# Kernel tuning notes

Hardware: AMD Instinct MI355X
Metric: run time of the kernel (lower is better)

Reference implementation:

```python
import jax, jax.numpy as jnp
import numpy as np

T_STEPS = 64   # rollout horizon (static for lax.scan)
DT = 0.1       # step(x, u) = x + DT*u (single-integrator dynamics)

def setup_inputs() -> dict:
    key = jax.random.key(0)
    k0, k1, k2, k3 = jax.random.split(key, 4)
    B, N, p, q, kgnn, fgnn = 64, 1024, 4, 4, 3, 32
    x0 = jax.random.normal(k0, (B, N, p), dtype=jnp.float32)
    # scale S so spectral norm ~O(1): matrix powers S^i stay bounded
    S = jax.random.normal(k1, (N, N), dtype=jnp.float32) / np.float32(np.sqrt(N))
    H1 = jax.random.normal(k2, (kgnn + 1, p, fgnn), dtype=jnp.float32)
    H2 = jax.random.normal(k3, (1, fgnn, q), dtype=jnp.float32)
    return {"x0": x0, "S": S, "H1": H1, "H2": H2}

def reference(x0, S, H1, H2):
    kgnn = H1.shape[0] - 1
    N = S.shape[0]
    # Precompute S^0..S^kgnn once (the torch code recomputes them every step)
    pows = [jnp.eye(N, dtype=S.dtype)]
    for _ in range(kgnn):
        pows.append(pows[-1] @ S)
    S_pows = jnp.stack(pows)  # (kgnn+1, N, N)

    def body(xt, _):
        # Z = tanh(sum_i S^i X H1[i]); each S^i @ X is a skinny matmul (inner dim p)
        SX = jnp.einsum('knm,bmp->kbnp', S_pows, xt)        # (k+1, B, N, p)
        Z = jnp.tanh(jnp.einsum('kbnp,kpf->bnf', SX, H1))   # (B, N, fgnn)
        U = jnp.einsum('nm,bmf,fq->bnq', S, Z, H2[0])       # (B, N, q)
        xn = xt + DT * U                                     # step(xt, ut)
        return xn, (xn, U)

    _, (xs, us) = jax.lax.scan(body, x0, None, length=T_STEPS)
    x_traj = jnp.concatenate([x0[:, None], jnp.moveaxis(xs, 0, 1)], axis=1)  # (B, T+1, N, p)
    u_traj = jnp.moveaxis(us, 0, 1)                                          # (B, T, N, q)
    return (x_traj, u_traj)
```

## Files before the change

kernel.cpp:

```cpp
#include <hip/hip_runtime.h>

#define T_STEPS 64
#define NN 1024
#define BKC 128

typedef __bf16 bf16x8 __attribute__((ext_vector_type(8)));
typedef float f32x4 __attribute__((ext_vector_type(4)));

__device__ __forceinline__ float fast_tanh(float z) {
    z = fminf(15.f, fmaxf(-15.f, z));
    const float t = __builtin_amdgcn_exp2f(z * 2.8853900817779268f);
    return (t - 1.f) * __builtin_amdgcn_rcpf(t + 1.f);
}

__global__ __launch_bounds__(512, 1) void step_kernel(
    const __bf16* __restrict__ AF,
    const __bf16* __restrict__ WFh, const __bf16* __restrict__ WFl,
    __bf16* __restrict__ WFoh, __bf16* __restrict__ WFol,
    float* __restrict__ SX, float* __restrict__ x_traj, float* __restrict__ u_traj,
    const float* __restrict__ H1, const float* __restrict__ H2, int t)
{
    __shared__ __align__(16) float dumps[8][4096];
    __shared__ float h1s[512];
    __shared__ float h2s[128];

    const int tid  = threadIdx.x;
    const int lane = tid & 63;
    const int w    = tid >> 6;

    h1s[tid & 511] = H1[tid & 511];
    if (tid < 128) h2s[tid] = H2[tid];

    const int l = blockIdx.x;
    const int xcd = l & 7, j = l >> 3;
    const int nb = xcd * 8 + (j & 7);
    const int cb = j >> 3;

    const __bf16* Abase  = AF  + ((size_t)nb * 32 + w * 4) * 4096 + lane * 8;
    const __bf16* Bbaseh = WFh + ((size_t)(cb * 4) * 32 + w * 4) * 512 + lane * 8;
    const __bf16* Bbasel = WFl + ((size_t)(cb * 4) * 32 + w * 4) * 512 + lane * 8;

    f32x4 acc[4][4];
    #pragma unroll
    for (int p = 0; p < 4; ++p)
        #pragma unroll
        for (int c = 0; c < 4; ++c)
            acc[p][c] = (f32x4){0.f, 0.f, 0.f, 0.f};

    #pragma unroll
    for (int kb = 0; kb < 4; ++kb) {
        bf16x8 ah[4], al[4], bh[4], bl[4];
        #pragma unroll
        for (int p = 0; p < 4; ++p) {
            ah[p] = *(const bf16x8*)(Abase + kb * 4096 + p * 512);
            al[p] = *(const bf16x8*)(Abase + kb * 4096 + 2048 + p * 512);
        }
        #pragma unroll
        for (int c = 0; c < 4; ++c) {
            bh[c] = *(const bf16x8*)(Bbaseh + kb * 512 + c * 16384);
            bl[c] = *(const bf16x8*)(Bbasel + kb * 512 + c * 16384);
        }
        #pragma unroll
        for (int p = 0; p < 4; ++p)
            #pragma unroll
            for (int c = 0; c < 4; ++c) {
                acc[p][c] = __builtin_amdgcn_mfma_f32_16x16x32_bf16(ah[p], bh[c], acc[p][c], 0, 0, 0);
                acc[p][c] = __builtin_amdgcn_mfma_f32_16x16x32_bf16(al[p], bh[c], acc[p][c], 0, 0, 0);
                acc[p][c] = __builtin_amdgcn_mfma_f32_16x16x32_bf16(ah[p], bl[c], acc[p][c], 0, 0, 0);
            }
    }

    #pragma unroll
    for (int p = 0; p < 4; ++p)
        #pragma unroll
        for (int c = 0; c < 4; ++c)
            *(f32x4*)&dumps[w][(p * 4 + c) * 256 + lane * 4] = acc[p][c];
    __syncthreads();
    {
        f32x4 s0 = *(const f32x4*)&dumps[0][tid * 8];
        f32x4 s1 = *(const f32x4*)&dumps[0][tid * 8 + 4];
        #pragma unroll
        for (int w2 = 1; w2 < 8; ++w2) {
            s0 += *(const f32x4*)&dumps[w2][tid * 8];
            s1 += *(const f32x4*)&dumps[w2][tid * 8 + 4];
        }
        *(f32x4*)&dumps[0][tid * 8] = s0;
        *(f32x4*)&dumps[0][tid * 8 + 4] = s1;
    }
    __syncthreads();

    if (tid < 256) {
        const int i  = tid & 15;
        const int bl2 = tid >> 4;
        const int n  = nb * 16 + i;
        const int bg = cb * 16 + bl2;
        const int rc = bl2 >> 2;
        const int lidx = ((i >> 2) << 4) + (bl2 & 3) * 4;
        const int rr = i & 3;

        float nv[4][4];
        f32x4 xv, uv;
        #pragma unroll
        for (int p = 0; p < 4; ++p) {
            f32x4 inc;
            #pragma unroll
            for (int q = 0; q < 4; ++q)
                inc[q] = dumps[0][(p * 4 + rc) * 256 + (lidx + q) * 4 + rr];
            const size_t so = (size_t)(p * NN + n) * 256 + bg * 4;
            f32x4 old = *(const f32x4*)(SX + so);
            f32x4 nw;
            #pragma unroll
            for (int q = 0; q < 4; ++q) nw[q] = fmaf(0.1f, inc[q], old[q]);
            *(f32x4*)(SX + so) = nw;
            #pragma unroll
            for (int q = 0; q < 4; ++q) nv[p][q] = nw[q];
            if (p == 0) { xv = nw; uv = inc; }
        }
        *(f32x4*)(x_traj + ((size_t)bg * (T_STEPS + 1) + t + 1) * 4096 + n * 4) = xv;
        *(f32x4*)(u_traj + ((size_t)bg * T_STEPS + t) * 4096 + n * 4) = uv;

        float w4[4] = {0.f, 0.f, 0.f, 0.f};
        #pragma unroll 4
        for (int f = 0; f < 32; ++f) {
            float z = 0.f;
            #pragma unroll
            for (int k = 0; k < 4; ++k)
                #pragma unroll
                for (int q = 0; q < 4; ++q)
                    z = fmaf(nv[k][q], h1s[(k * 4 + q) * 32 + f], z);
            z = fast_tanh(z);
            #pragma unroll
            for (int q = 0; q < 4; ++q) w4[q] = fmaf(z, h2s[f * 4 + q], w4[q]);
        }
        const int kblkw = n >> 5;
        const int lhi = ((n >> 3) & 3) << 4;
        const int jw = n & 7;
        #pragma unroll
        for (int q = 0; q < 4; ++q) {
            const int col = bg * 4 + q;
            const size_t o = ((size_t)(col >> 4) * 32 + kblkw) * 512 + ((col & 15) + lhi) * 8 + jw;
            const __bf16 h = (__bf16)w4[q];
            WFoh[o] = h;
            WFol[o] = (__bf16)(w4[q] - (float)h);
        }
    }
}

template<int MODE>
__global__ __launch_bounds__(256) void gemm_core(
    const __bf16* __restrict__ Ah, const __bf16* __restrict__ Al,
    const __bf16* __restrict__ Bh, const __bf16* __restrict__ Bl,
    __bf16* __restrict__ Oh, __bf16* __restrict__ Ol,
    float* __restrict__ SX)
{
    const int cb = blockIdx.x, nb = blockIdx.y;
    const int c0 = cb * 64;

    __shared__ char sA[2][16384];
    __shared__ char sB[2][16384];

    const int tid = threadIdx.x;
    const int lane = tid & 63;
    const int wid  = tid >> 6;
    const int wr = wid >> 1, wc = wid & 1;

    f32x4 acc[2][2];
    #pragma unroll
    for (int a = 0; a < 2; ++a)
        #pragma unroll
        for (int b = 0; b < 2; ++b)
            acc[a][b] = (f32x4){0.f, 0.f, 0.f, 0.f};

    for (int ch = 0; ch < 1024 / BKC; ++ch) {
        const int k0 = ch * BKC;
        __syncthreads();
        #pragma unroll
        for (int jj = 0; jj < 4; ++jj) {
            const int idx = jj * 256 + tid;
            const int r = idx >> 4, s = idx & 15;
            const int d = (r << 8) + ((s << 4) ^ ((r & 15) << 4));
            const int gA = nb * 64 + r;
            {
                const size_t off = (size_t)gA * 1024 + k0 + s * 8;
                *(uint4*)(sA[0] + d) = *(const uint4*)(Ah + off);
                *(uint4*)(sA[1] + d) = *(const uint4*)(Al + off);
            }
            {
                const size_t off = (size_t)(c0 + r) * 1024 + k0 + s * 8;
                *(uint4*)(sB[0] + d) = *(const uint4*)(Bh + off);
                *(uint4*)(sB[1] + d) = *(const uint4*)(Bl + off);
            }
        }
        __syncthreads();
        #pragma unroll
        for (int ks = 0; ks < 4; ++ks) {
            const int kb = ks * 64 + ((lane >> 4) << 4);
            bf16x8 afr[2][2], bfr[2][2];
            #pragma unroll
            for (int rt = 0; rt < 2; ++rt) {
                const int row = wr * 32 + rt * 16 + (lane & 15);
                const int d = (row << 8) + (kb ^ ((row & 15) << 4));
                afr[rt][0] = *(const bf16x8*)(sA[0] + d);
                afr[rt][1] = *(const bf16x8*)(sA[1] + d);
            }
            #pragma unroll
            for (int ct = 0; ct < 2; ++ct) {
                const int row = wc * 32 + ct * 16 + (lane & 15);
                const int d = (row << 8) + (kb ^ ((row & 15) << 4));
                bfr[ct][0] = *(const bf16x8*)(sB[0] + d);
                bfr[ct][1] = *(const bf16x8*)(sB[1] + d);
            }
            #pragma unroll
            for (int rt = 0; rt < 2; ++rt)
                #pragma unroll
                for (int ct = 0; ct < 2; ++ct) {
                    acc[rt][ct] = __builtin_amdgcn_mfma_f32_16x16x32_bf16(afr[rt][0], bfr[ct][0], acc[rt][ct], 0, 0, 0);
                    acc[rt][ct] = __builtin_amdgcn_mfma_f32_16x16x32_bf16(afr[rt][0], bfr[ct][1], acc[rt][ct], 0, 0, 0);
                    acc[rt][ct] = __builtin_amdgcn_mfma_f32_16x16x32_bf16(afr[rt][1], bfr[ct][0], acc[rt][ct], 0, 0, 0);
                }
        }
    }

    #pragma unroll
    for (int rt = 0; rt < 2; ++rt)
        #pragma unroll
        for (int ct = 0; ct < 2; ++ct)
            #pragma unroll
            for (int r = 0; r < 4; ++r) {
                const int row = wr * 32 + rt * 16 + ((lane >> 4) << 2) + r;
                const int col = wc * 32 + ct * 16 + (lane & 15);
                const float v = acc[rt][ct][r];
                if (MODE == 0) {
                    const size_t o = (size_t)(nb * 64 + row) * 1024 + c0 + col;
                    const __bf16 h = (__bf16)v;
                    Oh[o] = h;
                    Ol[o] = (__bf16)(v - (float)h);
                } else {
                    SX[(size_t)(nb * 64 + row) * 256 + c0 + col] = v;
                }
            }
}

__global__ __launch_bounds__(1024) void split_S(const float* __restrict__ S,
    __bf16* __restrict__ Ah, __bf16* __restrict__ Al,
    __bf16* __restrict__ STh, __bf16* __restrict__ STl)
{
    __shared__ float tile[32][33];
    const int tx = threadIdx.x & 31, ty = threadIdx.x >> 5;
    const int r0 = blockIdx.y * 32, c0 = blockIdx.x * 32;
    const float v = S[(size_t)(r0 + ty) * 1024 + c0 + tx];
    tile[ty][tx] = v;
    {
        const __bf16 h = (__bf16)v;
        const size_t o = (size_t)(r0 + ty) * 1024 + c0 + tx;
        Ah[o] = h; Al[o] = (__bf16)(v - (float)h);
    }
    __syncthreads();
    const float wv = tile[tx][ty];
    const __bf16 h = (__bf16)wv;
    const size_t o = (size_t)(c0 + ty) * 1024 + r0 + tx;
    STh[o] = h; STl[o] = (__bf16)(wv - (float)h);
}

__global__ __launch_bounds__(256) void repackAF2(const __bf16* __restrict__ rmh,
    const __bf16* __restrict__ rml, __bf16* __restrict__ AF)
{
    const int g = blockIdx.x * 256 + threadIdx.x;
    const int row = g >> 7;
    const int k0 = (g & 127) * 8;
    const int p = row >> 10, n = row & 1023;
    const int nb = n >> 4, i = n & 15;
    const int kblk = k0 >> 5, khi = (k0 >> 3) & 3;
    const size_t off = ((size_t)nb * 32 + kblk) * 4096 + p * 512 + (i + 16 * khi) * 8;
    *(bf16x8*)(AF + off)        = *(const bf16x8*)(rmh + (size_t)row * 1024 + k0);
    *(bf16x8*)(AF + off + 2048) = *(const bf16x8*)(rml + (size_t)row * 1024 + k0);
}

__global__ __launch_bounds__(256) void init_x0(const float* __restrict__ x0,
    float* __restrict__ SX, float* __restrict__ x_traj,
    __bf16* __restrict__ X0Th, __bf16* __restrict__ X0Tl)
{
    const int g = blockIdx.x * 256 + threadIdx.x;
    const int b = g >> 10, n = g & 1023;
    const f32x4 v = *(const f32x4*)(x0 + (size_t)g * 4);
    *(f32x4*)(SX + (size_t)n * 256 + b * 4) = v;
    *(f32x4*)(x_traj + (size_t)b * ((T_STEPS + 1) * 4096) + n * 4) = v;
    #pragma unroll
    for (int p = 0; p < 4; ++p) {
        const __bf16 h = (__bf16)v[p];
        const size_t o = (size_t)(b * 4 + p) * 1024 + n;
        X0Th[o] = h; X0Tl[o] = (__bf16)(v[p] - (float)h);
    }
}

__global__ __launch_bounds__(256) void w0_kernel(const float* __restrict__ SX,
    const float* __restrict__ H1, const float* __restrict__ H2,
    __bf16* __restrict__ WFh, __bf16* __restrict__ WFl)
{
    __shared__ float h1s[512], h2s[128];
    const int tid = threadIdx.x;
    for (int i2 = tid; i2 < 512; i2 += 256) h1s[i2] = H1[i2];
    if (tid < 128) h2s[tid] = H2[tid];
    __syncthreads();
    const int g = blockIdx.x * 256 + tid;
    const int b = g >> 10, n = g & 1023;
    float sx[16];
    #pragma unroll
    for (int k = 0; k < 4; ++k) {
        const f32x4 v = *(const f32x4*)(SX + (size_t)(k * NN + n) * 256 + b * 4);
        #pragma unroll
        for (int q = 0; q < 4; ++q) sx[k * 4 + q] = v[q];
    }
    float w4[4] = {0.f, 0.f, 0.f, 0.f};
    #pragma unroll 4
    for (int f = 0; f < 32; ++f) {
        float z = 0.f;
        #pragma unroll
        for (int kp = 0; kp < 16; ++kp) z = fmaf(sx[kp], h1s[kp * 32 + f], z);
        z = fast_tanh(z);
        #pragma unroll
        for (int q = 0; q < 4; ++q) w4[q] = fmaf(z, h2s[f * 4 + q], w4[q]);
    }
    const int kblkw = n >> 5;
    const int lhi = ((n >> 3) & 3) << 4;
    const int jw = n & 7;
    #pragma unroll
    for (int q = 0; q < 4; ++q) {
        const int col = b * 4 + q;
        const size_t o = ((size_t)(col >> 4) * 32 + kblkw) * 512 + ((col & 15) + lhi) * 8 + jw;
        const __bf16 h = (__bf16)w4[q];
        WFh[o] = h;
        WFl[o] = (__bf16)(w4[q] - (float)h);
    }
}

extern "C" void kernel_launch(void* const* d_in, const int* in_sizes, int n_in,
                              void* d_out, int out_size, void* d_ws, size_t ws_size,
                              hipStream_t stream)
{
    const float* x0 = (const float*)d_in[0];
    const float* S  = (const float*)d_in[1];
    const float* H1 = (const float*)d_in[2];
    const float* H2 = (const float*)d_in[3];

    float* x_traj = (float*)d_out;
    float* u_traj = x_traj + (size_t)64 * (T_STEPS + 1) * NN * 4;

    char* w = (char*)d_ws;
    __bf16* Ah_rm = (__bf16*)(w);
    __bf16* Al_rm = (__bf16*)(w + (8u << 20));
    __bf16* AF    = (__bf16*)(w + (16u << 20));
    float*  SX    = (float*) (w + (32u << 20));
    __bf16* WF0h  = (__bf16*)(w + (36u << 20));
    __bf16* WF0l  = (__bf16*)(w + (36u << 20) + (512u << 10));
    __bf16* WF1h  = (__bf16*)(w + (37u << 20));
    __bf16* WF1l  = (__bf16*)(w + (37u << 20) + (512u << 10));
    __bf16* STh   = AF;
    __bf16* STl   = AF + (size_t)1024 * 1024;
    __bf16* X0Th  = WF1h;
    __bf16* X0Tl  = WF1l;

    dim3 blk(256);

    split_S<<<dim3(32, 32), 1024, 0, stream>>>(S, Ah_rm, Al_rm, STh, STl);

    for (int jj = 1; jj <= 3; ++jj) {
        gemm_core<0><<<dim3(16, 16), blk, 0, stream>>>(
            Ah_rm + (size_t)(jj - 1) * 1024 * 1024, Al_rm + (size_t)(jj - 1) * 1024 * 1024,
            STh, STl,
            Ah_rm + (size_t)jj * 1024 * 1024, Al_rm + (size_t)jj * 1024 * 1024, nullptr);
    }

    init_x0<<<dim3(256), blk, 0, stream>>>(x0, SX, x_traj, X0Th, X0Tl);

    gemm_core<1><<<dim3(4, 48), blk, 0, stream>>>(
        Ah_rm, Al_rm, X0Th, X0Tl, nullptr, nullptr, SX + (size_t)1024 * 256);

    repackAF2<<<dim3(2048), blk, 0, stream>>>(Ah_rm, Al_rm, AF);

    w0_kernel<<<dim3(256), blk, 0, stream>>>(SX, H1, H2, WF0h, WF0l);

    for (int t = 0; t < T_STEPS; ++t) {
        const __bf16* rh = (t & 1) ? WF1h : WF0h;
        const __bf16* rl = (t & 1) ? WF1l : WF0l;
        __bf16* oh = (t & 1) ? WF0h : WF1h;
        __bf16* ol = (t & 1) ? WF0l : WF1l;
        step_kernel<<<dim3(256), dim3(512), 0, stream>>>(
            AF, rh, rl, oh, ol, SX, x_traj, u_traj, H1, H2, t);
    }
}
```

Measured before the change: 964.5 us.

## Fuse 64 step launches into one persistent kernel with grid barrier

Replaces the per-timestep kernel launches with a single persistent kernel that loops over all 64 steps and synchronises the 256 blocks through an atomic-counter grid barrier. The SX state is now held in registers across steps instead of being read and written in global memory each step. This is meant to remove launch overhead and the SX global traffic. In exchange it requires all 256 blocks to be co-resident, which risks deadlock if they are not, and adds spin-wait barrier latency.

```diff
diff --git a/kernel.cpp b/kernel.cpp
--- a/kernel.cpp
+++ b/kernel.cpp
@@ -13,12 +13,14 @@
     return (t - 1.f) * __builtin_amdgcn_rcpf(t + 1.f);
 }
 
-__global__ __launch_bounds__(512, 1) void step_kernel(
+__global__ __launch_bounds__(512, 1) void rollout(
     const __bf16* __restrict__ AF,
-    const __bf16* __restrict__ WFh, const __bf16* __restrict__ WFl,
-    __bf16* __restrict__ WFoh, __bf16* __restrict__ WFol,
-    float* __restrict__ SX, float* __restrict__ x_traj, float* __restrict__ u_traj,
-    const float* __restrict__ H1, const float* __restrict__ H2, int t)
+    __bf16* __restrict__ WF0h, __bf16* __restrict__ WF0l,
+    __bf16* __restrict__ WF1h, __bf16* __restrict__ WF1l,
+    const float* __restrict__ SX,
+    float* __restrict__ x_traj, float* __restrict__ u_traj,
+    const float* __restrict__ H1, const float* __restrict__ H2,
+    unsigned* __restrict__ ctr)
 {
     __shared__ __align__(16) float dumps[8][4096];
     __shared__ float h1s[512];
@@ -36,112 +38,142 @@
     const int nb = xcd * 8 + (j & 7);
     const int cb = j >> 3;
 
-    const __bf16* Abase  = AF  + ((size_t)nb * 32 + w * 4) * 4096 + lane * 8;
-    const __bf16* Bbaseh = WFh + ((size_t)(cb * 4) * 32 + w * 4) * 512 + lane * 8;
-    const __bf16* Bbasel = WFl + ((size_t)(cb * 4) * 32 + w * 4) * 512 + lane * 8;
-
-    f32x4 acc[4][4];
-    #pragma unroll
-    for (int p = 0; p < 4; ++p)
-        #pragma unroll
-        for (int c = 0; c < 4; ++c)
-            acc[p][c] = (f32x4){0.f, 0.f, 0.f, 0.f};
-
-    #pragma unroll
-    for (int kb = 0; kb < 4; ++kb) {
-        bf16x8 ah[4], al[4], bh[4], bl[4];
+    const __bf16* Abase = AF + ((size_t)nb * 32 + w * 4) * 4096 + lane * 8;
+    const size_t boff = ((size_t)(cb * 4) * 32 + w * 4) * 512 + lane * 8;
+
+    const int i   = tid & 15;
+    const int bl2 = (tid >> 4) & 15;
+    const int n   = nb * 16 + i;
+    const int bg  = cb * 16 + bl2;
+    const int rc  = bl2 >> 2;
+    const int lidx = ((i >> 2) << 4) + (bl2 & 3) * 4;
+    const int rr  = i & 3;
+    const int kblkw = n >> 5;
+    const int lhi = ((n >> 3) & 3) << 4;
+    const int jw  = n & 7;
+
+    float nv[4][4];
+    if (tid < 256) {
         #pragma unroll
         for (int p = 0; p < 4; ++p) {
-            ah[p] = *(const bf16x8*)(Abase + kb * 4096 + p * 512);
-            al[p] = *(const bf16x8*)(Abase + kb * 4096 + 2048 + p * 512);
-        }
-        #pragma unroll
-        for (int c = 0; c < 4; ++c) {
-            bh[c] = *(const bf16x8*)(Bbaseh + kb * 512 + c * 16384);
-            bl[c] = *(const bf16x8*)(Bbasel + kb * 512 + c * 16384);
-        }
+            const f32x4 v = *(const f32x4*)(SX + (size_t)(p * NN + n) * 256 + bg * 4);
+            #pragma unroll
+            for (int q = 0; q < 4; ++q) nv[p][q] = v[q];
+        }
+    }
+    __syncthreads();
+
+    unsigned bar = 0;
+
+    #pragma unroll 1
+    for (int t = 0; t < T_STEPS; ++t) {
+        const __bf16* Bbaseh = ((t & 1) ? WF1h : WF0h) + boff;
+        const __bf16* Bbasel = ((t & 1) ? WF1l : WF0l) + boff;
+        __bf16* Woh = (t & 1) ? WF0h : WF1h;
+        __bf16* Wol = (t & 1) ? WF0l : WF1l;
+
+        f32x4 acc[4][4];
         #pragma unroll
         for (int p = 0; p < 4; ++p)
             #pragma unroll
+            for (int c = 0; c < 4; ++c)
+                acc[p][c] = (f32x4){0.f, 0.f, 0.f, 0.f};
+
+        #pragma unroll
+        for (int kb = 0; kb < 4; ++kb) {
+            bf16x8 ah[4], al[4], bh[4], bl[4];
+            #pragma unroll
+            for (int p = 0; p < 4; ++p) {
+                ah[p] = *(const bf16x8*)(Abase + kb * 4096 + p * 512);
+                al[p] = *(const bf16x8*)(Abase + kb * 4096 + 2048 + p * 512);
+            }
+            #pragma unroll
             for (int c = 0; c < 4; ++c) {
-                acc[p][c] = __builtin_amdgcn_mfma_f32_16x16x32_bf16(ah[p], bh[c], acc[p][c], 0, 0, 0);
-                acc[p][c] = __builtin_amdgcn_mfma_f32_16x16x32_bf16(al[p], bh[c], acc[p][c], 0, 0, 0);
-                acc[p][c] = __builtin_amdgcn_mfma_f32_16x16x32_bf16(ah[p], bl[c], acc[p][c], 0, 0, 0);
-            }
-    }
-
-    #pragma unroll
-    for (int p = 0; p < 4; ++p)
-        #pragma unroll
-        for (int c = 0; c < 4; ++c)
-            *(f32x4*)&dumps[w][(p * 4 + c) * 256 + lane * 4] = acc[p][c];
-    __syncthreads();
-    {
-        f32x4 s0 = *(const f32x4*)&dumps[0][tid * 8];
-        f32x4 s1 = *(const f32x4*)&dumps[0][tid * 8 + 4];
-        #pragma unroll
-        for (int w2 = 1; w2 < 8; ++w2) {
-            s0 += *(const f32x4*)&dumps[w2][tid * 8];
-            s1 += *(const f32x4*)&dumps[w2][tid * 8 + 4];
-        }
-        *(f32x4*)&dumps[0][tid * 8] = s0;
-        *(f32x4*)&dumps[0][tid * 8 + 4] = s1;
-    }
-    __syncthreads();
-
-    if (tid < 256) {
-        const int i  = tid & 15;
-        const int bl2 = tid >> 4;
-        const int n  = nb * 16 + i;
-        const int bg = cb * 16 + bl2;
-        const int rc = bl2 >> 2;
-        const int lidx = ((i >> 2) << 4) + (bl2 & 3) * 4;
-        const int rr = i & 3;
-
-        float nv[4][4];
-        f32x4 xv, uv;
-        #pragma unroll
-        for (int p = 0; p < 4; ++p) {
-            f32x4 inc;
-            #pragma unroll
-            for (int q = 0; q < 4; ++q)
-                inc[q] = dumps[0][(p * 4 + rc) * 256 + (lidx + q) * 4 + rr];
-            const size_t so = (size_t)(p * NN + n) * 256 + bg * 4;
-            f32x4 old = *(const f32x4*)(SX + so);
-            f32x4 nw;
-            #pragma unroll
-            for (int q = 0; q < 4; ++q) nw[q] = fmaf(0.1f, inc[q], old[q]);
-            *(f32x4*)(SX + so) = nw;
-            #pragma unroll
-            for (int q = 0; q < 4; ++q) nv[p][q] = nw[q];
-            if (p == 0) { xv = nw; uv = inc; }
-        }
-        *(f32x4*)(x_traj + ((size_t)bg * (T_STEPS + 1) + t + 1) * 4096 + n * 4) = xv;
-        *(f32x4*)(u_traj + ((size_t)bg * T_STEPS + t) * 4096 + n * 4) = uv;
-
-        float w4[4] = {0.f, 0.f, 0.f, 0.f};
-        #pragma unroll 4
-        for (int f = 0; f < 32; ++f) {
-            float z = 0.f;
-            #pragma unroll
-            for (int k = 0; k < 4; ++k)
+                bh[c] = *(const bf16x8*)(Bbaseh + kb * 512 + c * 16384);
+                bl[c] = *(const bf16x8*)(Bbasel + kb * 512 + c * 16384);
+            }
+            #pragma unroll
+            for (int p = 0; p < 4; ++p)
+                #pragma unroll
+                for (int c = 0; c < 4; ++c) {
+                    acc[p][c] = __builtin_amdgcn_mfma_f32_16x16x32_bf16(ah[p], bh[c], acc[p][c], 0, 0, 0);
+                    acc[p][c] = __builtin_amdgcn_mfma_f32_16x16x32_bf16(al[p], bh[c], acc[p][c], 0, 0, 0);
+                    acc[p][c] = __builtin_amdgcn_mfma_f32_16x16x32_bf16(ah[p], bl[c], acc[p][c], 0, 0, 0);
+                }
+        }
+
+        #pragma unroll
+        for (int p = 0; p < 4; ++p)
+            #pragma unroll
+            for (int c = 0; c < 4; ++c)
+                *(f32x4*)&dumps[w][(p * 4 + c) * 256 + lane * 4] = acc[p][c];
+        __syncthreads();
+        {
+            f32x4 s0 = *(const f32x4*)&dumps[0][tid * 8];
+            f32x4 s1 = *(const f32x4*)&dumps[0][tid * 8 + 4];
+            #pragma unroll
+            for (int w2 = 1; w2 < 8; ++w2) {
+                s0 += *(const f32x4*)&dumps[w2][tid * 8];
+                s1 += *(const f32x4*)&dumps[w2][tid * 8 + 4];
+            }
+            *(f32x4*)&dumps[0][tid * 8] = s0;
+            *(f32x4*)&dumps[0][tid * 8 + 4] = s1;
+        }
+        __syncthreads();
+
+        if (tid < 256) {
+            f32x4 xv, uv;
+            #pragma unroll
+            for (int p = 0; p < 4; ++p) {
+                f32x4 inc;
                 #pragma unroll
                 for (int q = 0; q < 4; ++q)
-                    z = fmaf(nv[k][q], h1s[(k * 4 + q) * 32 + f], z);
-            z = fast_tanh(z);
-            #pragma unroll
-            for (int q = 0; q < 4; ++q) w4[q] = fmaf(z, h2s[f * 4 + q], w4[q]);
-        }
-        const int kblkw = n >> 5;
-        const int lhi = ((n >> 3) & 3) << 4;
-        const int jw = n & 7;
-        #pragma unroll
-        for (int q = 0; q < 4; ++q) {
-            const int col = bg * 4 + q;
-            const size_t o = ((size_t)(col >> 4) * 32 + kblkw) * 512 + ((col & 15) + lhi) * 8 + jw;
-            const __bf16 h = (__bf16)w4[q];
-            WFoh[o] = h;
-            WFol[o] = (__bf16)(w4[q] - (float)h);
+                    inc[q] = dumps[0][(p * 4 + rc) * 256 + (lidx + q) * 4 + rr];
+                #pragma unroll
+                for (int q = 0; q < 4; ++q) nv[p][q] = fmaf(0.1f, inc[q], nv[p][q]);
+                if (p == 0) {
+                    #pragma unroll
+                    for (int q = 0; q < 4; ++q) { xv[q] = nv[0][q]; uv[q] = inc[q]; }
+                }
+            }
+            *(f32x4*)(x_traj + ((size_t)bg * (T_STEPS + 1) + t + 1) * 4096 + n * 4) = xv;
+            *(f32x4*)(u_traj + ((size_t)bg * T_STEPS + t) * 4096 + n * 4) = uv;
+
+            float w4[4] = {0.f, 0.f, 0.f, 0.f};
+            #pragma unroll 4
+            for (int f = 0; f < 32; ++f) {
+                float z = 0.f;
+                #pragma unroll
+                for (int k = 0; k < 4; ++k)
+                    #pragma unroll
+                    for (int q = 0; q < 4; ++q)
+                        z = fmaf(nv[k][q], h1s[(k * 4 + q) * 32 + f], z);
+                z = fast_tanh(z);
+                #pragma unroll
+                for (int q = 0; q < 4; ++q) w4[q] = fmaf(z, h2s[f * 4 + q], w4[q]);
+            }
+            #pragma unroll
+            for (int q = 0; q < 4; ++q) {
+                const int col = bg * 4 + q;
+                const size_t o = ((size_t)(col >> 4) * 32 + kblkw) * 512 + ((col & 15) + lhi) * 8 + jw;
+                const __bf16 h = (__bf16)w4[q];
+                Woh[o] = h;
+                Wol[o] = (__bf16)(w4[q] - (float)h);
+            }
+        }
+
+        if (t < T_STEPS - 1) {
+            __syncthreads();
+            if (tid == 0) {
+                __threadfence();
+                __hip_atomic_fetch_add(ctr, 1u, __ATOMIC_RELEASE, __HIP_MEMORY_SCOPE_AGENT);
+                const unsigned tgt = bar + 256;
+                while (__hip_atomic_load(ctr, __ATOMIC_ACQUIRE, __HIP_MEMORY_SCOPE_AGENT) < tgt)
+                    __builtin_amdgcn_s_sleep(2);
+                __threadfence();
+            }
+            bar += 256;
+            __syncthreads();
         }
     }
 }
@@ -355,6 +387,7 @@
     __bf16* WF0l  = (__bf16*)(w + (36u << 20) + (512u << 10));
     __bf16* WF1h  = (__bf16*)(w + (37u << 20));
     __bf16* WF1l  = (__bf16*)(w + (37u << 20) + (512u << 10));
+    unsigned* ctr = (unsigned*)(w + (4u << 20));
     __bf16* STh   = AF;
     __bf16* STl   = AF + (size_t)1024 * 1024;
     __bf16* X0Th  = WF1h;
@@ -380,12 +413,7 @@
 
     w0_kernel<<<dim3(256), blk, 0, stream>>>(SX, H1, H2, WF0h, WF0l);
 
-    for (int t = 0; t < T_STEPS; ++t) {
-        const __bf16* rh = (t & 1) ? WF1h : WF0h;
-        const __bf16* rl = (t & 1) ? WF1l : WF0l;
-        __bf16* oh = (t & 1) ? WF0h : WF1h;
-        __bf16* ol = (t & 1) ? WF0l : WF1l;
-        step_kernel<<<dim3(256), dim3(512), 0, stream>>>(
-            AF, rh, rl, oh, ol, SX, x_traj, u_traj, H1, H2, t);
-    }
-}
+    hipMemsetAsync(ctr, 0, 256, stream);
+    rollout<<<dim3(256), dim3(512), 0, stream>>>(
+        AF, WF0h, WF0l, WF1h, WF1l, SX, x_traj, u_traj, H1, H2, ctr);
+}
```

Result: slower. 2.876 ms (+198.2%).

## Split K across two wave groups with double-buffered loads and smaller LDS reduction

Applied to the files above, without the earlier changes.

The MFMA work is repartitioned so each wave owns one column quadrant and half of the K range, instead of every wave owning all columns and one eighth of K. Operand loads are double-buffered across 16 K steps. The cross-wave reduction shrinks from eight partial tiles to two, using a padded 64x68 LDS layout. Trajectory outputs now use nontemporal stores. The cost is fewer independent accumulators per wave and a longer serial MFMA chain per wave, in exchange for less LDS traffic and less reduction work.

```diff
diff --git a/kernel.cpp b/kernel.cpp
--- a/kernel.cpp
+++ b/kernel.cpp
@@ -11,6 +11,10 @@
     z = fminf(15.f, fmaxf(-15.f, z));
     const float t = __builtin_amdgcn_exp2f(z * 2.8853900817779268f);
     return (t - 1.f) * __builtin_amdgcn_rcpf(t + 1.f);
+}
+
+__device__ __forceinline__ void nt_store4(float* p, f32x4 v) {
+    __builtin_nontemporal_store(v, (f32x4*)p);
 }
 
 __global__ __launch_bounds__(512, 1) void step_kernel(
@@ -20,13 +24,15 @@
     float* __restrict__ SX, float* __restrict__ x_traj, float* __restrict__ u_traj,
     const float* __restrict__ H1, const float* __restrict__ H2, int t)
 {
-    __shared__ __align__(16) float dumps[8][4096];
+    __shared__ __align__(16) float dumps[2][64][68];
     __shared__ float h1s[512];
     __shared__ float h2s[128];
 
     const int tid  = threadIdx.x;
     const int lane = tid & 63;
     const int w    = tid >> 6;
+    const int ks   = w >> 2;
+    const int cq   = w & 3;
 
     h1s[tid & 511] = H1[tid & 511];
     if (tid < 128) h2s[tid] = H2[tid];
@@ -36,76 +42,75 @@
     const int nb = xcd * 8 + (j & 7);
     const int cb = j >> 3;
 
-    const __bf16* Abase  = AF  + ((size_t)nb * 32 + w * 4) * 4096 + lane * 8;
-    const __bf16* Bbaseh = WFh + ((size_t)(cb * 4) * 32 + w * 4) * 512 + lane * 8;
-    const __bf16* Bbasel = WFl + ((size_t)(cb * 4) * 32 + w * 4) * 512 + lane * 8;
-
-    f32x4 acc[4][4];
-    #pragma unroll
-    for (int p = 0; p < 4; ++p)
-        #pragma unroll
-        for (int c = 0; c < 4; ++c)
-            acc[p][c] = (f32x4){0.f, 0.f, 0.f, 0.f};
-
-    #pragma unroll
-    for (int kb = 0; kb < 4; ++kb) {
-        bf16x8 ah[4], al[4], bh[4], bl[4];
+    const __bf16* Abase  = AF  + ((size_t)nb * 32 + ks * 16) * 4096 + lane * 8;
+    const __bf16* Bbaseh = WFh + ((size_t)(cb * 4 + cq) * 32 + ks * 16) * 512 + lane * 8;
+    const __bf16* Bbasel = WFl + ((size_t)(cb * 4 + cq) * 32 + ks * 16) * 512 + lane * 8;
+
+    f32x4 acc[4];
+    #pragma unroll
+    for (int p = 0; p < 4; ++p) acc[p] = (f32x4){0.f, 0.f, 0.f, 0.f};
+
+    bf16x8 ah[2][4], al[2][4], bh[2], bl[2];
+    #pragma unroll
+    for (int p = 0; p < 4; ++p) {
+        ah[0][p] = *(const bf16x8*)(Abase + p * 512);
+        al[0][p] = *(const bf16x8*)(Abase + 2048 + p * 512);
+    }
+    bh[0] = *(const bf16x8*)(Bbaseh);
+    bl[0] = *(const bf16x8*)(Bbasel);
+
+    #pragma unroll
+    for (int kb = 0; kb < 16; ++kb) {
+        const int cur = kb & 1, nxt = cur ^ 1;
+        if (kb < 15) {
+            #pragma unroll
+            for (int p = 0; p < 4; ++p) {
+                ah[nxt][p] = *(const bf16x8*)(Abase + (kb + 1) * 4096 + p * 512);
+                al[nxt][p] = *(const bf16x8*)(Abase + (kb + 1) * 4096 + 2048 + p * 512);
+            }
+            bh[nxt] = *(const bf16x8*)(Bbaseh + (kb + 1) * 512);
+            bl[nxt] = *(const bf16x8*)(Bbasel + (kb + 1) * 512);
+        }
         #pragma unroll
         for (int p = 0; p < 4; ++p) {
-            ah[p] = *(const bf16x8*)(Abase + kb * 4096 + p * 512);
-            al[p] = *(const bf16x8*)(Abase + kb * 4096 + 2048 + p * 512);
-        }
-        #pragma unroll
-        for (int c = 0; c < 4; ++c) {
-            bh[c] = *(const bf16x8*)(Bbaseh + kb * 512 + c * 16384);
-            bl[c] = *(const bf16x8*)(Bbasel + kb * 512 + c * 16384);
-        }
+            acc[p] = __builtin_amdgcn_mfma_f32_16x16x32_bf16(ah[cur][p], bh[cur], acc[p], 0, 0, 0);
+            acc[p] = __builtin_amdgcn_mfma_f32_16x16x32_bf16(al[cur][p], bh[cur], acc[p], 0, 0, 0);
+            acc[p] = __builtin_amdgcn_mfma_f32_16x16x32_bf16(ah[cur][p], bl[cur], acc[p], 0, 0, 0);
+        }
+    }
+
+    {
+        const int rbase = (lane >> 4) * 4;
+        const int c = cq * 16 + (lane & 15);
         #pragma unroll
         for (int p = 0; p < 4; ++p)
             #pragma unroll
-            for (int c = 0; c < 4; ++c) {
-                acc[p][c] = __builtin_amdgcn_mfma_f32_16x16x32_bf16(ah[p], bh[c], acc[p][c], 0, 0, 0);
-                acc[p][c] = __builtin_amdgcn_mfma_f32_16x16x32_bf16(al[p], bh[c], acc[p][c], 0, 0, 0);
-                acc[p][c] = __builtin_amdgcn_mfma_f32_16x16x32_bf16(ah[p], bl[c], acc[p][c], 0, 0, 0);
-            }
-    }
-
-    #pragma unroll
-    for (int p = 0; p < 4; ++p)
-        #pragma unroll
-        for (int c = 0; c < 4; ++c)
-            *(f32x4*)&dumps[w][(p * 4 + c) * 256 + lane * 4] = acc[p][c];
+            for (int r = 0; r < 4; ++r)
+                dumps[ks][p * 16 + rbase + r][c] = acc[p][r];
+    }
     __syncthreads();
     {
-        f32x4 s0 = *(const f32x4*)&dumps[0][tid * 8];
-        f32x4 s1 = *(const f32x4*)&dumps[0][tid * 8 + 4];
-        #pragma unroll
-        for (int w2 = 1; w2 < 8; ++w2) {
-            s0 += *(const f32x4*)&dumps[w2][tid * 8];
-            s1 += *(const f32x4*)&dumps[w2][tid * 8 + 4];
-        }
-        *(f32x4*)&dumps[0][tid * 8] = s0;
-        *(f32x4*)&dumps[0][tid * 8 + 4] = s1;
+        const int row = tid >> 3, cg = (tid & 7) * 8;
+        f32x4 s0 = *(const f32x4*)&dumps[0][row][cg];
+        f32x4 s1 = *(const f32x4*)&dumps[0][row][cg + 4];
+        s0 += *(const f32x4*)&dumps[1][row][cg];
+        s1 += *(const f32x4*)&dumps[1][row][cg + 4];
+        *(f32x4*)&dumps[0][row][cg]     = s0;
+        *(f32x4*)&dumps[0][row][cg + 4] = s1;
     }
     __syncthreads();
 
     if (tid < 256) {
-        const int i  = tid & 15;
+        const int i   = tid & 15;
         const int bl2 = tid >> 4;
-        const int n  = nb * 16 + i;
-        const int bg = cb * 16 + bl2;
-        const int rc = bl2 >> 2;
-        const int lidx = ((i >> 2) << 4) + (bl2 & 3) * 4;
-        const int rr = i & 3;
+        const int n   = nb * 16 + i;
+        const int bg  = cb * 16 + bl2;
 
         float nv[4][4];
         f32x4 xv, uv;
         #pragma unroll
         for (int p = 0; p < 4; ++p) {
-            f32x4 inc;
-            #pragma unroll
-            for (int q = 0; q < 4; ++q)
-                inc[q] = dumps[0][(p * 4 + rc) * 256 + (lidx + q) * 4 + rr];
+            const f32x4 inc = *(const f32x4*)&dumps[0][p * 16 + i][bl2 * 4];
             const size_t so = (size_t)(p * NN + n) * 256 + bg * 4;
             f32x4 old = *(const f32x4*)(SX + so);
             f32x4 nw;
@@ -116,8 +121,8 @@
             for (int q = 0; q < 4; ++q) nv[p][q] = nw[q];
             if (p == 0) { xv = nw; uv = inc; }
         }
-        *(f32x4*)(x_traj + ((size_t)bg * (T_STEPS + 1) + t + 1) * 4096 + n * 4) = xv;
-        *(f32x4*)(u_traj + ((size_t)bg * T_STEPS + t) * 4096 + n * 4) = uv;
+        nt_store4(x_traj + ((size_t)bg * (T_STEPS + 1) + t + 1) * 4096 + n * 4, xv);
+        nt_store4(u_traj + ((size_t)bg * T_STEPS + t) * 4096 + n * 4, uv);
 
         float w4[4] = {0.f, 0.f, 0.f, 0.f};
         #pragma unroll 4
```

Result: slower. 1.289 ms (+33.6%).
